# Kernel optimization log

Hardware: AMD Instinct MI355X
Metric: run time of the kernel (lower is better)

The kernel has to match this reference:

```python
import jax, jax.numpy as jnp
import numpy as np

B, C, H, W = 8, 256, 128, 128
NH, WS = 8, 8
HD = C // NH
WNH, WNW = H // WS, W // WS


def _rel_pos_index():
    coords = np.stack(np.meshgrid(np.arange(WS), np.arange(WS), indexing='ij'))  # [2,ws,ws]
    flat = coords.reshape(2, -1)
    rel = (flat[:, :, None] - flat[:, None, :]).transpose(1, 2, 0)  # [ws^2,ws^2,2]
    rel[..., 0] += WS - 1
    rel[..., 1] += WS - 1
    rel[..., 0] *= 2 * WS - 1
    return jnp.asarray(rel.sum(-1))  # [ws^2,ws^2]


def grid_sample(img, grid):
    # Bilinear, padding_mode='zeros', align_corners=True. img [N,C,H,W], grid [N,Hg,Wg,2] (x,y in [-1,1])
    N, Ci, Hi, Wi = img.shape
    gx = (grid[..., 0] + 1.0) * 0.5 * (Wi - 1)
    gy = (grid[..., 1] + 1.0) * 0.5 * (Hi - 1)
    x0 = jnp.floor(gx)
    y0 = jnp.floor(gy)
    x0i = x0.astype(jnp.int32)
    y0i = y0.astype(jnp.int32)
    wx1 = gx - x0
    wx0 = 1.0 - wx1
    wy1 = gy - y0
    wy0 = 1.0 - wy1
    nb = jnp.arange(N)[:, None, None]

    def corner(yi, xi, wgt):
        valid = (yi >= 0) & (yi < Hi) & (xi >= 0) & (xi < Wi)
        yc = jnp.clip(yi, 0, Hi - 1)
        xc = jnp.clip(xi, 0, Wi - 1)
        val = img[nb, :, yc, xc]  # [N,Hg,Wg,C]
        return val * (wgt * valid)[..., None]

    out = (corner(y0i, x0i, wy0 * wx0) + corner(y0i, x0i + 1, wy0 * wx1)
           + corner(y0i + 1, x0i, wy1 * wx0) + corner(y0i + 1, x0i + 1, wy1 * wx1))
    return jnp.transpose(out, (0, 3, 1, 2))


def setup_inputs() -> dict:
    key = jax.random.key(0)
    ks = jax.random.split(key, 10)
    f = lambda k, s, sc=1.0: jax.random.normal(k, s, dtype=jnp.float32) * sc
    return {
        'x': f(ks[0], (B, C, H, W)),
        'qkv_w': f(ks[1], (3 * C, C), 0.02),
        'qkv_b': f(ks[2], (3 * C,), 0.02),
        'bias_w': f(ks[3], (2 * NH, C), 0.02),
        'bias_b': f(ks[4], (2 * NH,), 0.02),
        'scale_w': f(ks[5], (2 * NH, C), 0.02),
        'scale_b': f(ks[6], (2 * NH,), 0.02),
        'proj_w': f(ks[7], (C, C), 0.02),
        'proj_b': f(ks[8], (C,), 0.02),
        'rpb_table': f(ks[9], ((2 * WS - 1) ** 2, NH), 0.02),
    }


def reference(x, qkv_w, qkv_b, bias_w, bias_b, scale_w, scale_b, proj_w, proj_b, rpb_table):
    scale = HD ** -0.5
    N = B * NH
    # ---- deterministic base sampling coordinates (shift=0, no padding since H,W % WS == 0) ----
    lin_w = jnp.linspace(-1.0, 1.0, W)
    lin_h = jnp.linspace(-1.0, 1.0, H)
    winref_w = lin_w.reshape(WNW, WS).mean(-1)  # window centers along width
    winref_h = lin_h.reshape(WNH, WS).mean(-1)
    off_w = jnp.arange(WS) * 2.0 / (W - 1)
    off_w = off_w - off_w.mean()
    off_h = jnp.arange(WS) * 2.0 / (H - 1)
    off_h = off_h - off_h.mean()
    base_x = jnp.broadcast_to(winref_w[None, None, :, None] + off_w[None, None, None, :], (WNH, WS, WNW, WS))
    base_y = jnp.broadcast_to((winref_h[:, None] + off_h[None, :])[:, :, None, None], (WNH, WS, WNW, WS))
    # ---- predicted per-head per-window biases & scales ----
    xp = jax.nn.leaky_relu(x.reshape(B, C, WNH, WS, WNW, WS).mean((3, 5)))  # [B,C,WNH,WNW]
    biases = (jnp.einsum('oc,bchw->bohw', bias_w, xp) + bias_b[None, :, None, None]).reshape(N, 2, WNH, WNW)
    bx = biases[:, 0] / WNW  # sampling_biases[:,0] / (w // ws)
    by = biases[:, 1] / WNH
    scales = (jnp.einsum('oc,bchw->bohw', scale_w, xp) + scale_b[None, :, None, None]).reshape(N, 2, WNH, WNW)
    sx, sy = scales[:, 0], scales[:, 1]
    # final = base + local_offsets * scale + bias (broadcast [N,WNH,1,WNW,1] over window interior)
    cx = base_x[None] + off_w[None, None, None, None, :] * sx[:, :, None, :, None] + bx[:, :, None, :, None]
    cy = base_y[None] + off_h[None, None, :, None, None] * sy[:, :, None, :, None] + by[:, :, None, :, None]
    grid = jnp.stack([cx, cy], -1).reshape(N, H, W, 2)
    # ---- qkv via 1x1 conv ----
    qkv = (jnp.einsum('oc,bchw->bohw', qkv_w, x) + qkv_b[None, :, None, None]).reshape(B, 3, NH, HD, H, W)
    q = qkv[:, 0].reshape(N, HD, H, W)
    k = qkv[:, 1].reshape(N, HD, H, W)
    v = qkv[:, 2].reshape(N, HD, H, W)
    ksamp = grid_sample(k, grid)
    vsamp = grid_sample(v, grid)

    def win(t):  # [N,HD,H,W] -> [B, nWin, NH, WS*WS, HD]
        t = t.reshape(B, NH, HD, WNH, WS, WNW, WS)
        return jnp.transpose(t, (0, 3, 5, 1, 4, 6, 2)).reshape(B, WNH * WNW, NH, WS * WS, HD)

    qw, kw, vw = win(q), win(ksamp), win(vsamp)
    rpb = jnp.transpose(rpb_table[_rel_pos_index().reshape(-1)].reshape(WS * WS, WS * WS, NH), (2, 0, 1))
    attn = jnp.einsum('bwhqd,bwhkd->bwhqk', qw, kw) * scale + rpb[None, None]
    attn = jax.nn.softmax(attn, axis=-1)
    out = jnp.einsum('bwhqk,bwhkd->bwhqd', attn, vw)
    out = out.reshape(B, WNH, WNW, NH, WS, WS, HD)
    out = jnp.transpose(out, (0, 3, 6, 1, 4, 2, 5)).reshape(B, C, H, W)
    out = jnp.einsum('oc,bchw->bohw', proj_w, out) + proj_b[None, :, None, None]
    return out
```

## Files before the change

kernel.cpp:

```cpp
#include <hip/hip_runtime.h>
#include <hip/hip_fp16.h>

#define B_ 8
#define C_ 256
#define H_ 128
#define W_ 128
#define NH_ 8
#define WS_ 8
#define HD_ 32
#define WN_ 16
#define NWIN_ 256
#define HW_ 16384

typedef unsigned short ushort_t;
typedef unsigned int uint_t;
typedef __attribute__((ext_vector_type(8))) short short8;
typedef _Float16 __attribute__((ext_vector_type(8))) half8;
typedef __attribute__((ext_vector_type(4))) float f32x4;

__device__ __forceinline__ ushort_t bf16_rtn(float x) {
    uint_t u = __float_as_uint(x);
    return (ushort_t)((u + 0x7FFFu + ((u >> 16) & 1u)) >> 16);
}
__device__ __forceinline__ uint_t bfpack(float a, float b) {
    return (uint_t)bf16_rtn(a) | ((uint_t)bf16_rtn(b) << 16);
}
__device__ __forceinline__ uint_t h2pack(float a, float b) {
    __half2 h = __floats2half2_rn(a, b);
    return __builtin_bit_cast(uint_t, h);
}

__global__ __launch_bounds__(256) void wconv_kernel(const float* __restrict__ w,
                            ushort_t* __restrict__ wh, int n4) {
    int i = blockIdx.x*256 + threadIdx.x;
    if (i >= n4) return;
    float4 v = ((const float4*)w)[i];
    ((uint2*)wh)[i] = make_uint2(bfpack(v.x, v.y), bfpack(v.z, v.w));
}

__global__ __launch_bounds__(256) void rpb_expand_kernel(const float* __restrict__ rpb_table,
                            float* __restrict__ rpbT) {
    int nh = blockIdx.x;
    int t = threadIdx.x;
    #pragma unroll
    for (int rr = 0; rr < 16; ++rr) {
        int e = t*16 + rr;
        int kcol = e >> 6, qrow = e & 63;
        int yq = qrow >> 3, xq = qrow & 7, yk = kcol >> 3, xk = kcol & 7;
        int idx = (yq - yk + 7)*15 + (xq - xk + 7);
        rpbT[((size_t)nh*64 + kcol)*64 + qrow] = rpb_table[idx*8 + nh];
    }
}

__global__ __launch_bounds__(256) void transpose_split_kernel(const float* __restrict__ x,
                            ushort_t* __restrict__ th, float* __restrict__ xpart) {
    __shared__ float tile[64][65];
    int b = blockIdx.z;
    int p0 = blockIdx.x * 64, c0 = blockIdx.y * 64;
    const float* xsrc = x + (size_t)b*C_*HW_;
    int t = threadIdx.x;
    #pragma unroll
    for (int r = 0; r < 4; ++r) {
        int task = t + r*256;
        int cl = task >> 4, p4 = (task & 15) * 4;
        float4 v = *(const float4*)(xsrc + (size_t)(c0+cl)*HW_ + p0 + p4);
        tile[cl][p4+0] = v.x; tile[cl][p4+1] = v.y; tile[cl][p4+2] = v.z; tile[cl][p4+3] = v.w;
    }
    __syncthreads();
    {
        int h = blockIdx.x >> 1, wbase = (blockIdx.x & 1) * 8;
        #pragma unroll
        for (int r = 0; r < 2; ++r) {
            int task = t + r*256;
            int cl = task >> 3, wx = task & 7;
            float s = 0.f;
            #pragma unroll
            for (int j = 0; j < 8; ++j) s += tile[cl][wx*8+j];
            xpart[(((size_t)b*256 + c0+cl)*128 + h)*16 + wbase + wx] = s;
        }
    }
    ushort_t* thb = th + (size_t)b*HW_*256;
    #pragma unroll
    for (int r = 0; r < 2; ++r) {
        int task = t + r*256;
        int pl = task >> 3, cb = (task & 7) * 8;
        uint4 Hh;
        Hh.x = bfpack(tile[cb+0][pl], tile[cb+1][pl]);
        Hh.y = bfpack(tile[cb+2][pl], tile[cb+3][pl]);
        Hh.z = bfpack(tile[cb+4][pl], tile[cb+5][pl]);
        Hh.w = bfpack(tile[cb+6][pl], tile[cb+7][pl]);
        *(uint4*)(thb + (size_t)(p0+pl)*256 + c0 + cb) = Hh;
    }
}

__global__ __launch_bounds__(256) void pool2_kernel(const float* __restrict__ xpart, float* __restrict__ xp) {
    int bc = blockIdx.x;
    int t = threadIdx.x;
    int wy = t >> 4, wxg = t & 15;
    const float* src = xpart + (size_t)bc*2048;
    float s = 0.f;
    #pragma unroll
    for (int i = 0; i < 8; ++i) s += src[(wy*8+i)*16 + wxg];
    s *= (1.f/64.f);
    xp[(size_t)bc*256 + t] = s > 0.f ? s : 0.01f*s;
}

__global__ __launch_bounds__(256) void params_kernel(const float* __restrict__ xp,
                              const float* __restrict__ bias_w, const float* __restrict__ bias_b,
                              const float* __restrict__ scale_w, const float* __restrict__ scale_b,
                              float* __restrict__ params) {
    __shared__ float xs[256];
    int blk = blockIdx.x;
    int b = blk >> 8, win = blk & 255;
    int t = threadIdx.x;
    xs[t] = xp[((size_t)(b*256 + t))*256 + win];
    __syncthreads();
    if (t < 32) {
        int which = t >> 4;
        int o = t & 15;
        const float* Wm = which ? scale_w : bias_w;
        float acc = which ? scale_b[o] : bias_b[o];
        for (int c = 0; c < 256; ++c) acc += Wm[o*256 + c] * xs[c];
        int nh = o >> 1, comp = o & 1;
        int n = b*8 + nh;
        float v = which ? acc : 3.96875f * acc;
        params[((size_t)(n*256 + win))*4 + which*2 + comp] = v;
    }
}

__global__ __launch_bounds__(256) void mgemm_qkvt_kernel(const ushort_t* __restrict__ wq,
                            const ushort_t* __restrict__ xt,
                            const float* __restrict__ bias,
                            ushort_t* __restrict__ qt, ushort_t* __restrict__ kv) {
    __shared__ __align__(16) uint4 smem[2112];
    uint4* Ah = smem; uint4* Bh = smem + 1024;
    int zb = blockIdx.z;
    const ushort_t* xh = xt + (size_t)zb*HW_*256;
    ushort_t* qtb = qt + (size_t)zb*HW_*256;
    ushort_t* kvb = kv + (size_t)zb*8*HW_*64;
    int o0 = blockIdx.x * 128, p0 = blockIdx.y * 128;
    int t = threadIdx.x;
    int lane = t & 63, wid = t >> 6;
    int wm = wid >> 1, wn = wid & 1;
    int q = lane >> 4, rl = lane & 15;

    f32x4 acc[4][4];
    #pragma unroll
    for (int f = 0; f < 4; ++f)
        #pragma unroll
        for (int g = 0; g < 4; ++g)
            acc[f][g] = (f32x4){0.f, 0.f, 0.f, 0.f};

    int srow = t >> 1, shalf = t & 1;
    int sw = srow & 7;

    for (int ks = 0; ks < 4; ++ks) {
        int c0 = ks * 64;
        __syncthreads();
        {
            const uint4* a_h = (const uint4*)(wq + (size_t)(o0+srow)*256 + c0);
            const uint4* b_h = (const uint4*)(xh + (size_t)(p0+srow)*256 + c0);
            #pragma unroll
            for (int jj = 0; jj < 4; ++jj) {
                int u = shalf*4 + jj;
                int d = srow*8 + (u ^ sw);
                Ah[d] = a_h[u]; Bh[d] = b_h[u];
            }
        }
        __syncthreads();
        #pragma unroll
        for (int kk = 0; kk < 2; ++kk) {
            short8 afh[4], bfh[4];
            #pragma unroll
            for (int f = 0; f < 4; ++f) {
                int row = wm*64 + f*16 + rl;
                int u = (kk*4 + q) ^ (row & 7);
                afh[f] = __builtin_bit_cast(short8, Ah[row*8 + u]);
            }
            #pragma unroll
            for (int g = 0; g < 4; ++g) {
                int row = wn*64 + g*16 + rl;
                int u = (kk*4 + q) ^ (row & 7);
                bfh[g] = __builtin_bit_cast(short8, Bh[row*8 + u]);
            }
            #pragma unroll
            for (int f = 0; f < 4; ++f)
                #pragma unroll
                for (int g = 0; g < 4; ++g)
                    acc[f][g] = __builtin_amdgcn_mfma_f32_16x16x32_bf16(afh[f], bfh[g], acc[f][g], 0, 0, 0);
        }
    }
    float* tb = (float*)smem;
    int pl = t >> 1, half = t & 1;
    #pragma unroll
    for (int pass = 0; pass < 2; ++pass) {
        __syncthreads();
        if (wm == pass) {
            #pragma unroll
            for (int f = 0; f < 4; ++f)
                #pragma unroll
                for (int g = 0; g < 4; ++g)
                    #pragma unroll
                    for (int r = 0; r < 4; ++r)
                        tb[(f*16 + q*4 + r)*129 + wn*64 + g*16 + rl] = acc[f][g][r];
        }
        __syncthreads();
        {
            int obase = o0 + pass*64 + half*32;
            int type = obase >> 8;
            int oo = obase & 255;
            int head = oo >> 5;
            size_t pix = p0 + pl;
            ushort_t* dst = (type == 0)
                ? qtb + pix*256 + oo
                : kvb + ((size_t)head*HW_ + pix)*64 + ((type == 2) ? 32 : 0) + (oo & 31);
            #pragma unroll
            for (int u = 0; u < 4; ++u) {
                float v[8];
                #pragma unroll
                for (int e = 0; e < 8; ++e) v[e] = tb[(half*32 + u*8 + e)*129 + pl];
                float4 b0 = *(const float4*)&bias[obase + u*8];
                float4 b1 = *(const float4*)&bias[obase + u*8 + 4];
                uint4 Hv;
                Hv.x = h2pack(v[0]+b0.x, v[1]+b0.y);
                Hv.y = h2pack(v[2]+b0.z, v[3]+b0.w);
                Hv.z = h2pack(v[4]+b1.x, v[5]+b1.y);
                Hv.w = h2pack(v[6]+b1.z, v[7]+b1.w);
                *(uint4*)(dst + u*8) = Hv;
            }
        }
    }
}

__global__ __launch_bounds__(256) void mgemm_proj_kernel(const ushort_t* __restrict__ wp,
                            const ushort_t* __restrict__ at,
                            const float* __restrict__ bias, float* __restrict__ out) {
    __shared__ __align__(16) uint4 smem[2048];
    uint4* Ah = smem; uint4* Bh = smem + 1024;
    int zb = blockIdx.z;
    const ushort_t* xh = at + (size_t)zb*HW_*256;
    float* outb = out + (size_t)zb*C_*HW_;
    int o0 = blockIdx.x * 128, p0 = blockIdx.y * 128;
    int t = threadIdx.x;
    int lane = t & 63, wid = t >> 6;
    int wm = wid >> 1, wn = wid & 1;
    int q = lane >> 4, rl = lane & 15;

    f32x4 acc[4][4];
    #pragma unroll
    for (int f = 0; f < 4; ++f)
        #pragma unroll
        for (int g = 0; g < 4; ++g)
            acc[f][g] = (f32x4){0.f, 0.f, 0.f, 0.f};

    int srow = t >> 1, shalf = t & 1;
    int sw = srow & 7;

    for (int ks = 0; ks < 4; ++ks) {
        int c0 = ks * 64;
        __syncthreads();
        {
            const uint4* a_h = (const uint4*)(wp + (size_t)(o0+srow)*256 + c0);
            const uint4* b_h = (const uint4*)(xh + (size_t)(p0+srow)*256 + c0);
            #pragma unroll
            for (int jj = 0; jj < 4; ++jj) {
                int u = shalf*4 + jj;
                int d = srow*8 + (u ^ sw);
                Ah[d] = a_h[u]; Bh[d] = b_h[u];
            }
        }
        __syncthreads();
        #pragma unroll
        for (int kk = 0; kk < 2; ++kk) {
            short8 afh[4], bfh[4];
            #pragma unroll
            for (int f = 0; f < 4; ++f) {
                int row = wm*64 + f*16 + rl;
                int u = (kk*4 + q) ^ (row & 7);
                afh[f] = __builtin_bit_cast(short8, Ah[row*8 + u]);
            }
            #pragma unroll
            for (int g = 0; g < 4; ++g) {
                int row = wn*64 + g*16 + rl;
                int u = (kk*4 + q) ^ (row & 7);
                bfh[g] = __builtin_bit_cast(short8, Bh[row*8 + u]);
            }
            #pragma unroll
            for (int f = 0; f < 4; ++f)
                #pragma unroll
                for (int g = 0; g < 4; ++g)
                    acc[f][g] = __builtin_amdgcn_mfma_f32_16x16x32_bf16(afh[f], bfh[g], acc[f][g], 0, 0, 0);
        }
    }
    #pragma unroll
    for (int f = 0; f < 4; ++f) {
        float4 bb = *(const float4*)&bias[o0 + wm*64 + f*16 + q*4];
        float bbv[4] = {bb.x, bb.y, bb.z, bb.w};
        #pragma unroll
        for (int g = 0; g < 4; ++g) {
            int p = p0 + wn*64 + g*16 + rl;
            #pragma unroll
            for (int r = 0; r < 4; ++r) {
                int o = o0 + wm*64 + f*16 + q*4 + r;
                outb[(size_t)o*HW_ + p] = acc[f][g][r] + bbv[r];
            }
        }
    }
}

__global__ __launch_bounds__(256) void attn_kernel(const ushort_t* __restrict__ qt,
                            const ushort_t* __restrict__ kv,
                            const float* __restrict__ params_,
                            const float* __restrict__ rpbT,
                            ushort_t* __restrict__ at) {
    __shared__ __align__(16) ushort_t smem[64*40 + 64*40 + 32*72 + 64*40];
    ushort_t (*Q_lds)[40]   = (ushort_t(*)[40])smem;
    ushort_t (*K_lds)[40]   = (ushort_t(*)[40])(smem + 2560);
    ushort_t (*VT_lds)[72]  = (ushort_t(*)[72])(smem + 5120);
    ushort_t (*P_lds)[72]   = (ushort_t(*)[72])smem;
    ushort_t (*OUT_lds)[40] = (ushort_t(*)[40])(smem + 5120 + 2304);

    int b = blockIdx.y;
    int blk = blockIdx.x;
    int win = blk >> 3, nh = blk & 7;
    int wy = win >> 4, wx = win & 15;
    int t = threadIdx.x;
    int lane = t & 63, wid = t >> 6;

    const float* pp = params_ + ((size_t)((b*8 + nh)*256 + win))*4;
    float ox = pp[0], oy = pp[1], sx = pp[2], sy = pp[3];

    const ushort_t* qtb = qt + (size_t)b*HW_*256;
    const ushort_t* kvb = kv + ((size_t)(b*8 + nh))*HW_*64;
    ushort_t* ath = at + (size_t)b*HW_*256;

    {
        int tok = t >> 2, cg = t & 3;
        int i = tok >> 3, j = tok & 7;
        size_t pix = (size_t)(wy*8 + i)*W_ + wx*8 + j;
        *(uint4*)&Q_lds[tok][cg*8] = *(const uint4*)(qtb + pix*256 + nh*32 + cg*8);
    }
    {
        int tokq = lane >> 3, sub = lane & 7;
        #pragma unroll
        for (int r = 0; r < 2; ++r) {
            int tok = wid*16 + r*8 + tokq;
            int i = tok >> 3, j = tok & 7;
            int h = wy*8 + i, wpx = wx*8 + j;
            float gx = (float)wpx + ((float)j - 3.5f)*sx + ox;
            float gy = (float)h  + ((float)i - 3.5f)*sy + oy;
            float x0f = floorf(gx), y0f = floorf(gy);
            int x0 = (int)x0f, y0 = (int)y0f;
            float wx1 = gx - x0f, wy1 = gy - y0f;
            float wxz = 1.f - wx1, wyz = 1.f - wy1;
            int x1 = x0 + 1, y1 = y0 + 1;
            float m00 = wyz*wxz * ((y0>=0 && y0<H_ && x0>=0 && x0<W_) ? 1.f : 0.f);
            float m01 = wyz*wx1 * ((y0>=0 && y0<H_ && x1>=0 && x1<W_) ? 1.f : 0.f);
            float m10 = wy1*wxz * ((y1>=0 && y1<H_ && x0>=0 && x0<W_) ? 1.f : 0.f);
            float m11 = wy1*wx1 * ((y1>=0 && y1<H_ && x1>=0 && x1<W_) ? 1.f : 0.f);
            int x0c = min(max(x0,0),W_-1), x1c = min(max(x1,0),W_-1);
            int y0c = min(max(y0,0),H_-1), y1c = min(max(y1,0),H_-1);
            size_t p00 = (size_t)y0c*W_ + x0c, p01 = (size_t)y0c*W_ + x1c;
            size_t p10 = (size_t)y1c*W_ + x0c, p11 = (size_t)y1c*W_ + x1c;
            __half2 a0 = __float2half2_rn(0.f), a1 = a0, a2 = a0, a3 = a0;
            #define CORNER(PIX, M) { \
                uint4 u = *(const uint4*)(kvb + (PIX)*64 + sub*8); \
                __half2 wv = __float2half2_rn(M); \
                a0 = __hfma2(__builtin_bit_cast(__half2, u.x), wv, a0); \
                a1 = __hfma2(__builtin_bit_cast(__half2, u.y), wv, a1); \
                a2 = __hfma2(__builtin_bit_cast(__half2, u.z), wv, a2); \
                a3 = __hfma2(__builtin_bit_cast(__half2, u.w), wv, a3); }
            CORNER(p00, m00)
            CORNER(p01, m01)
            CORNER(p10, m10)
            CORNER(p11, m11)
            #undef CORNER
            if (sub < 4) {
                uint4 Kv;
                Kv.x = __builtin_bit_cast(uint_t, a0); Kv.y = __builtin_bit_cast(uint_t, a1);
                Kv.z = __builtin_bit_cast(uint_t, a2); Kv.w = __builtin_bit_cast(uint_t, a3);
                *(uint4*)&K_lds[tok][sub*8] = Kv;
            } else {
                int d0 = (sub - 4)*8;
                VT_lds[d0+0][tok] = __half_as_ushort(__low2half(a0));
                VT_lds[d0+1][tok] = __half_as_ushort(__high2half(a0));
                VT_lds[d0+2][tok] = __half_as_ushort(__low2half(a1));
                VT_lds[d0+3][tok] = __half_as_ushort(__high2half(a1));
                VT_lds[d0+4][tok] = __half_as_ushort(__low2half(a2));
                VT_lds[d0+5][tok] = __half_as_ushort(__high2half(a2));
                VT_lds[d0+6][tok] = __half_as_ushort(__low2half(a3));
                VT_lds[d0+7][tok] = __half_as_ushort(__high2half(a3));
            }
        }
    }
    __syncthreads();

    int q = lane >> 4, rl = lane & 15;
    const float scale = 0.17677669529663687f;

    half8 a_frag = *(const half8*)&Q_lds[wid*16 + rl][q*8];
    half8 b_frag[4];
    #pragma unroll
    for (int g = 0; g < 4; ++g)
        b_frag[g] = *(const half8*)&K_lds[g*16 + rl][q*8];
    __syncthreads();

    f32x4 accS[4];
    #pragma unroll
    for (int g = 0; g < 4; ++g)
        accS[g] = __builtin_amdgcn_mfma_f32_16x16x32_f16(a_frag, b_frag[g], (f32x4){0.f,0.f,0.f,0.f}, 0, 0, 0);

    float Sv[4][4];
    const float* rpbb = rpbT + (size_t)nh*4096;
    int m0 = wid*16 + q*4;
    #pragma unroll
    for (int g = 0; g < 4; ++g) {
        float4 rv = *(const float4*)&rpbb[(g*16 + rl)*64 + m0];
        Sv[g][0] = accS[g][0]*scale + rv.x;
        Sv[g][1] = accS[g][1]*scale + rv.y;
        Sv[g][2] = accS[g][2]*scale + rv.z;
        Sv[g][3] = accS[g][3]*scale + rv.w;
    }
    float inv[4];
    #pragma unroll
    for (int r = 0; r < 4; ++r) {
        float pm = fmaxf(fmaxf(Sv[0][r], Sv[1][r]), fmaxf(Sv[2][r], Sv[3][r]));
        pm = fmaxf(pm, __shfl_xor(pm, 1));
        pm = fmaxf(pm, __shfl_xor(pm, 2));
        pm = fmaxf(pm, __shfl_xor(pm, 4));
        pm = fmaxf(pm, __shfl_xor(pm, 8));
        float s = 0.f;
        #pragma unroll
        for (int g = 0; g < 4; ++g) {
            float e = __expf(Sv[g][r] - pm);
            Sv[g][r] = e;
            s += e;
        }
        s += __shfl_xor(s, 1);
        s += __shfl_xor(s, 2);
        s += __shfl_xor(s, 4);
        s += __shfl_xor(s, 8);
        inv[r] = 1.f / s;
    }
    #pragma unroll
    for (int r = 0; r < 4; ++r) {
        int m = wid*16 + q*4 + r;
        #pragma unroll
        for (int g = 0; g < 4; ++g)
            P_lds[m][g*16 + rl] = __half_as_ushort(__float2half(Sv[g][r]*inv[r]));
    }

    f32x4 accO[2] = {(f32x4){0.f,0.f,0.f,0.f}, (f32x4){0.f,0.f,0.f,0.f}};
    #pragma unroll
    for (int ks = 0; ks < 2; ++ks) {
        half8 p_frag = *(const half8*)&P_lds[wid*16 + rl][ks*32 + q*8];
        #pragma unroll
        for (int g2 = 0; g2 < 2; ++g2) {
            half8 v_frag = *(const half8*)&VT_lds[g2*16 + rl][ks*32 + q*8];
            accO[g2] = __builtin_amdgcn_mfma_f32_16x16x32_f16(p_frag, v_frag, accO[g2], 0, 0, 0);
        }
    }
    #pragma unroll
    for (int r = 0; r < 4; ++r) {
        int m = wid*16 + q*4 + r;
        OUT_lds[m][rl]      = bf16_rtn(accO[0][r]);
        OUT_lds[m][16 + rl] = bf16_rtn(accO[1][r]);
    }
    __syncthreads();
    {
        int tok = t >> 2, cg = t & 3;
        int i2 = tok >> 3, j2 = tok & 7;
        size_t pix = (size_t)(wy*8 + i2)*W_ + wx*8 + j2;
        *(uint4*)(ath + pix*256 + nh*32 + cg*8) = *(const uint4*)&OUT_lds[tok][cg*8];
    }
}

extern "C" void kernel_launch(void* const* d_in, const int* in_sizes, int n_in,
                              void* d_out, int out_size, void* d_ws, size_t ws_size,
                              hipStream_t stream) {
    const float* x       = (const float*)d_in[0];
    const float* qkv_w   = (const float*)d_in[1];
    const float* qkv_b   = (const float*)d_in[2];
    const float* bias_w  = (const float*)d_in[3];
    const float* bias_b  = (const float*)d_in[4];
    const float* scale_w = (const float*)d_in[5];
    const float* scale_b = (const float*)d_in[6];
    const float* proj_w  = (const float*)d_in[7];
    const float* proj_b  = (const float*)d_in[8];
    const float* rpb     = (const float*)d_in[9];
    float* out = (float*)d_out;

    char* ws = (char*)d_ws;
    float*    xp       = (float*)ws;     ws += (size_t)524288*4;
    float*    params   = (float*)ws;     ws += (size_t)65536*4;
    float*    xpart    = (float*)ws;     ws += (size_t)4194304*4;
    float*    rpbT     = (float*)ws;     ws += (size_t)8*4096*4;
    ushort_t* wq       = (ushort_t*)ws;  ws += (size_t)768*256*2;
    ushort_t* wp       = (ushort_t*)ws;  ws += (size_t)256*256*2;
    ushort_t* xt       = (ushort_t*)ws;  ws += (size_t)B_*HW_*256*2;
    ushort_t* at       = (ushort_t*)ws;  ws += (size_t)B_*HW_*256*2;
    ushort_t* qt       = (ushort_t*)ws;  ws += (size_t)B_*HW_*256*2;
    ushort_t* kv       = (ushort_t*)ws;

    wconv_kernel<<<dim3(192), 256, 0, stream>>>(qkv_w, wq, 768*256/4);
    wconv_kernel<<<dim3(64),  256, 0, stream>>>(proj_w, wp, 256*256/4);
    rpb_expand_kernel<<<dim3(NH_), 256, 0, stream>>>(rpb, rpbT);
    transpose_split_kernel<<<dim3(256, 4, B_), 256, 0, stream>>>(x, xt, xpart);
    pool2_kernel <<<dim3(B_*C_), 256, 0, stream>>>(xpart, xp);
    params_kernel<<<dim3(B_*NWIN_), 256, 0, stream>>>(xp, bias_w, bias_b, scale_w, scale_b, params);
    mgemm_qkvt_kernel<<<dim3(6, 128, B_), 256, 0, stream>>>(wq, xt, qkv_b, qt, kv);
    attn_kernel<<<dim3(NH_*NWIN_, B_), 256, 0, stream>>>(qt, kv, params, rpbT, at);
    mgemm_proj_kernel<<<dim3(2, 128, B_), 256, 0, stream>>>(wp, at, proj_b, out);
}
```

Measured before the change: 361.0 us.

## Fuse x transpose and pooling partials into QKV GEMM with fp16 operands

```diff
diff --git a/kernel.cpp b/kernel.cpp
--- a/kernel.cpp
+++ b/kernel.cpp
@@ -30,6 +30,14 @@
     return __builtin_bit_cast(uint_t, h);
 }
 
+__global__ __launch_bounds__(256) void wconv_h_kernel(const float* __restrict__ w,
+                            ushort_t* __restrict__ wh, int n4) {
+    int i = blockIdx.x*256 + threadIdx.x;
+    if (i >= n4) return;
+    float4 v = ((const float4*)w)[i];
+    ((uint2*)wh)[i] = make_uint2(h2pack(v.x, v.y), h2pack(v.z, v.w));
+}
+
 __global__ __launch_bounds__(256) void wconv_kernel(const float* __restrict__ w,
                             ushort_t* __restrict__ wh, int n4) {
     int i = blockIdx.x*256 + threadIdx.x;
@@ -49,47 +57,6 @@
         int yq = qrow >> 3, xq = qrow & 7, yk = kcol >> 3, xk = kcol & 7;
         int idx = (yq - yk + 7)*15 + (xq - xk + 7);
         rpbT[((size_t)nh*64 + kcol)*64 + qrow] = rpb_table[idx*8 + nh];
-    }
-}
-
-__global__ __launch_bounds__(256) void transpose_split_kernel(const float* __restrict__ x,
-                            ushort_t* __restrict__ th, float* __restrict__ xpart) {
-    __shared__ float tile[64][65];
-    int b = blockIdx.z;
-    int p0 = blockIdx.x * 64, c0 = blockIdx.y * 64;
-    const float* xsrc = x + (size_t)b*C_*HW_;
-    int t = threadIdx.x;
-    #pragma unroll
-    for (int r = 0; r < 4; ++r) {
-        int task = t + r*256;
-        int cl = task >> 4, p4 = (task & 15) * 4;
-        float4 v = *(const float4*)(xsrc + (size_t)(c0+cl)*HW_ + p0 + p4);
-        tile[cl][p4+0] = v.x; tile[cl][p4+1] = v.y; tile[cl][p4+2] = v.z; tile[cl][p4+3] = v.w;
-    }
-    __syncthreads();
-    {
-        int h = blockIdx.x >> 1, wbase = (blockIdx.x & 1) * 8;
-        #pragma unroll
-        for (int r = 0; r < 2; ++r) {
-            int task = t + r*256;
-            int cl = task >> 3, wx = task & 7;
-            float s = 0.f;
-            #pragma unroll
-            for (int j = 0; j < 8; ++j) s += tile[cl][wx*8+j];
-            xpart[(((size_t)b*256 + c0+cl)*128 + h)*16 + wbase + wx] = s;
-        }
-    }
-    ushort_t* thb = th + (size_t)b*HW_*256;
-    #pragma unroll
-    for (int r = 0; r < 2; ++r) {
-        int task = t + r*256;
-        int pl = task >> 3, cb = (task & 7) * 8;
-        uint4 Hh;
-        Hh.x = bfpack(tile[cb+0][pl], tile[cb+1][pl]);
-        Hh.y = bfpack(tile[cb+2][pl], tile[cb+3][pl]);
-        Hh.z = bfpack(tile[cb+4][pl], tile[cb+5][pl]);
-        Hh.w = bfpack(tile[cb+6][pl], tile[cb+7][pl]);
-        *(uint4*)(thb + (size_t)(p0+pl)*256 + c0 + cb) = Hh;
     }
 }
 
@@ -128,17 +95,21 @@
     }
 }
 
-__global__ __launch_bounds__(256) void mgemm_qkvt_kernel(const ushort_t* __restrict__ wq,
-                            const ushort_t* __restrict__ xt,
+__global__ __launch_bounds__(256) void mgemm_qkvx_kernel(const ushort_t* __restrict__ wq,
+                            const float* __restrict__ x,
                             const float* __restrict__ bias,
-                            ushort_t* __restrict__ qt, ushort_t* __restrict__ kv) {
-    __shared__ __align__(16) uint4 smem[2112];
-    uint4* Ah = smem; uint4* Bh = smem + 1024;
+                            ushort_t* __restrict__ qt, ushort_t* __restrict__ kv,
+                            float* __restrict__ xpart) {
+    __shared__ __align__(16) uint4 Albuf[1024];
+    __shared__ __align__(16) float Btile[64*129];
+    uint4* B16 = (uint4*)Btile;
+
     int zb = blockIdx.z;
-    const ushort_t* xh = xt + (size_t)zb*HW_*256;
+    const float* xb = x + (size_t)zb*C_*HW_;
     ushort_t* qtb = qt + (size_t)zb*HW_*256;
     ushort_t* kvb = kv + (size_t)zb*8*HW_*64;
     int o0 = blockIdx.x * 128, p0 = blockIdx.y * 128;
+    int hrow = blockIdx.y;
     int t = threadIdx.x;
     int lane = t & 63, wid = t >> 6;
     int wm = wid >> 1, wn = wid & 1;
@@ -159,38 +130,76 @@
         __syncthreads();
         {
             const uint4* a_h = (const uint4*)(wq + (size_t)(o0+srow)*256 + c0);
-            const uint4* b_h = (const uint4*)(xh + (size_t)(p0+srow)*256 + c0);
             #pragma unroll
             for (int jj = 0; jj < 4; ++jj) {
                 int u = shalf*4 + jj;
-                int d = srow*8 + (u ^ sw);
-                Ah[d] = a_h[u]; Bh[d] = b_h[u];
-            }
+                Albuf[srow*8 + (u ^ sw)] = a_h[u];
+            }
+        }
+        {
+            #pragma unroll
+            for (int r = 0; r < 8; ++r) {
+                int task = t + r*256;
+                int cl = task >> 5, p4 = (task & 31) * 4;
+                float4 v = *(const float4*)(xb + (size_t)(c0+cl)*HW_ + p0 + p4);
+                float* dst = &Btile[cl*129 + p4];
+                dst[0] = v.x; dst[1] = v.y; dst[2] = v.z; dst[3] = v.w;
+            }
+        }
+        __syncthreads();
+        if (blockIdx.x == 0) {
+            #pragma unroll
+            for (int r = 0; r < 4; ++r) {
+                int task = t + r*256;
+                int cl = task >> 4, wxg = task & 15;
+                float s = 0.f;
+                #pragma unroll
+                for (int j = 0; j < 8; ++j) s += Btile[cl*129 + wxg*8 + j];
+                xpart[(((size_t)zb*256 + c0+cl)*128 + hrow)*16 + wxg] = s;
+            }
+        }
+        uint4 cvt[4];
+        #pragma unroll
+        for (int r = 0; r < 4; ++r) {
+            int task = t + r*256;
+            int pl = task >> 3, cb = (task & 7) * 8;
+            float f[8];
+            #pragma unroll
+            for (int e = 0; e < 8; ++e) f[e] = Btile[(cb+e)*129 + pl];
+            cvt[r].x = h2pack(f[0], f[1]); cvt[r].y = h2pack(f[2], f[3]);
+            cvt[r].z = h2pack(f[4], f[5]); cvt[r].w = h2pack(f[6], f[7]);
+        }
+        __syncthreads();
+        #pragma unroll
+        for (int r = 0; r < 4; ++r) {
+            int task = t + r*256;
+            int pl = task >> 3, u = task & 7;
+            B16[pl*8 + (u ^ (pl & 7))] = cvt[r];
         }
         __syncthreads();
         #pragma unroll
         for (int kk = 0; kk < 2; ++kk) {
-            short8 afh[4], bfh[4];
+            half8 afh[4], bfh[4];
             #pragma unroll
             for (int f = 0; f < 4; ++f) {
                 int row = wm*64 + f*16 + rl;
                 int u = (kk*4 + q) ^ (row & 7);
-                afh[f] = __builtin_bit_cast(short8, Ah[row*8 + u]);
+                afh[f] = __builtin_bit_cast(half8, Albuf[row*8 + u]);
             }
             #pragma unroll
             for (int g = 0; g < 4; ++g) {
                 int row = wn*64 + g*16 + rl;
                 int u = (kk*4 + q) ^ (row & 7);
-                bfh[g] = __builtin_bit_cast(short8, Bh[row*8 + u]);
+                bfh[g] = __builtin_bit_cast(half8, B16[row*8 + u]);
             }
             #pragma unroll
             for (int f = 0; f < 4; ++f)
                 #pragma unroll
                 for (int g = 0; g < 4; ++g)
-                    acc[f][g] = __builtin_amdgcn_mfma_f32_16x16x32_bf16(afh[f], bfh[g], acc[f][g], 0, 0, 0);
-        }
-    }
-    float* tb = (float*)smem;
+                    acc[f][g] = __builtin_amdgcn_mfma_f32_16x16x32_f16(afh[f], bfh[g], acc[f][g], 0, 0, 0);
+        }
+    }
+    float* tb = Btile;
     int pl = t >> 1, half = t & 1;
     #pragma unroll
     for (int pass = 0; pass < 2; ++pass) {
@@ -497,18 +506,16 @@
     float*    rpbT     = (float*)ws;     ws += (size_t)8*4096*4;
     ushort_t* wq       = (ushort_t*)ws;  ws += (size_t)768*256*2;
     ushort_t* wp       = (ushort_t*)ws;  ws += (size_t)256*256*2;
-    ushort_t* xt       = (ushort_t*)ws;  ws += (size_t)B_*HW_*256*2;
     ushort_t* at       = (ushort_t*)ws;  ws += (size_t)B_*HW_*256*2;
     ushort_t* qt       = (ushort_t*)ws;  ws += (size_t)B_*HW_*256*2;
     ushort_t* kv       = (ushort_t*)ws;
 
-    wconv_kernel<<<dim3(192), 256, 0, stream>>>(qkv_w, wq, 768*256/4);
-    wconv_kernel<<<dim3(64),  256, 0, stream>>>(proj_w, wp, 256*256/4);
+    wconv_h_kernel<<<dim3(192), 256, 0, stream>>>(qkv_w, wq, 768*256/4);
+    wconv_kernel  <<<dim3(64),  256, 0, stream>>>(proj_w, wp, 256*256/4);
     rpb_expand_kernel<<<dim3(NH_), 256, 0, stream>>>(rpb, rpbT);
-    transpose_split_kernel<<<dim3(256, 4, B_), 256, 0, stream>>>(x, xt, xpart);
+    mgemm_qkvx_kernel<<<dim3(6, 128, B_), 256, 0, stream>>>(wq, x, qkv_b, qt, kv, xpart);
     pool2_kernel <<<dim3(B_*C_), 256, 0, stream>>>(xpart, xp);
     params_kernel<<<dim3(B_*NWIN_), 256, 0, stream>>>(xp, bias_w, bias_b, scale_w, scale_b, params);
-    mgemm_qkvt_kernel<<<dim3(6, 128, B_), 256, 0, stream>>>(wq, xt, qkv_b, qt, kv);
     attn_kernel<<<dim3(NH_*NWIN_, B_), 256, 0, stream>>>(qt, kv, params, rpbT, at);
     mgemm_proj_kernel<<<dim3(2, 128, B_), 256, 0, stream>>>(wp, at, proj_b, out);
 }
```

Result: no change. 362.2 us (+0.3%).

## Pre-pack QKV weights in MFMA fragment order and load A directly from global

Applied to the files above, without the earlier changes.

```diff
diff --git a/kernel.cpp b/kernel.cpp
--- a/kernel.cpp
+++ b/kernel.cpp
@@ -28,6 +28,26 @@
 __device__ __forceinline__ uint_t h2pack(float a, float b) {
     __half2 h = __floats2half2_rn(a, b);
     return __builtin_bit_cast(uint_t, h);
+}
+
+__global__ __launch_bounds__(256) void wpack_kernel(const float* __restrict__ w,
+                            ushort_t* __restrict__ wpk) {
+    int u = blockIdx.x*256 + threadIdx.x;
+    int lane = u & 63;
+    int f    = (u >> 6) & 3;
+    int kk   = (u >> 8) & 1;
+    int ks   = (u >> 9) & 3;
+    int wm   = (u >> 11) & 1;
+    int oc   = u >> 12;
+    int o = oc*128 + wm*64 + f*16 + (lane & 15);
+    int c = ks*64 + kk*32 + (lane >> 4)*8;
+    const float* src = w + (size_t)o*256 + c;
+    float4 v0 = *(const float4*)src;
+    float4 v1 = *(const float4*)(src + 4);
+    uint4 Hv;
+    Hv.x = bfpack(v0.x, v0.y); Hv.y = bfpack(v0.z, v0.w);
+    Hv.z = bfpack(v1.x, v1.y); Hv.w = bfpack(v1.z, v1.w);
+    ((uint4*)wpk)[u] = Hv;
 }
 
 __global__ __launch_bounds__(256) void wconv_kernel(const float* __restrict__ w,
@@ -128,21 +148,25 @@
     }
 }
 
-__global__ __launch_bounds__(256) void mgemm_qkvt_kernel(const ushort_t* __restrict__ wq,
+__global__ __launch_bounds__(256) void mgemm_qkvt2_kernel(const ushort_t* __restrict__ wpk,
                             const ushort_t* __restrict__ xt,
                             const float* __restrict__ bias,
                             ushort_t* __restrict__ qt, ushort_t* __restrict__ kv) {
-    __shared__ __align__(16) uint4 smem[2112];
-    uint4* Ah = smem; uint4* Bh = smem + 1024;
+    __shared__ __align__(16) float smem_f[64*67];
+    uint4* Bh = (uint4*)smem_f;
+    float* tb = smem_f;
     int zb = blockIdx.z;
+    int oc = blockIdx.x;
+    int o0 = oc * 128, p0 = blockIdx.y * 128;
     const ushort_t* xh = xt + (size_t)zb*HW_*256;
     ushort_t* qtb = qt + (size_t)zb*HW_*256;
     ushort_t* kvb = kv + (size_t)zb*8*HW_*64;
-    int o0 = blockIdx.x * 128, p0 = blockIdx.y * 128;
     int t = threadIdx.x;
     int lane = t & 63, wid = t >> 6;
     int wm = wid >> 1, wn = wid & 1;
-    int q = lane >> 4, rl = lane & 15;
+    int qi = lane >> 4, rl = lane & 15;
+
+    const ushort_t* wpkA = wpk + (size_t)(oc*2 + wm)*16384;
 
     f32x4 acc[4][4];
     #pragma unroll
@@ -155,32 +179,27 @@
     int sw = srow & 7;
 
     for (int ks = 0; ks < 4; ++ks) {
-        int c0 = ks * 64;
         __syncthreads();
         {
-            const uint4* a_h = (const uint4*)(wq + (size_t)(o0+srow)*256 + c0);
-            const uint4* b_h = (const uint4*)(xh + (size_t)(p0+srow)*256 + c0);
+            const uint4* src = (const uint4*)(xh + (size_t)(p0+srow)*256 + ks*64);
             #pragma unroll
             for (int jj = 0; jj < 4; ++jj) {
                 int u = shalf*4 + jj;
-                int d = srow*8 + (u ^ sw);
-                Ah[d] = a_h[u]; Bh[d] = b_h[u];
+                Bh[srow*8 + (u ^ sw)] = src[u];
             }
         }
         __syncthreads();
         #pragma unroll
         for (int kk = 0; kk < 2; ++kk) {
             short8 afh[4], bfh[4];
-            #pragma unroll
-            for (int f = 0; f < 4; ++f) {
-                int row = wm*64 + f*16 + rl;
-                int u = (kk*4 + q) ^ (row & 7);
-                afh[f] = __builtin_bit_cast(short8, Ah[row*8 + u]);
-            }
+            const ushort_t* wk = wpkA + ((ks*2 + kk)*4)*512 + lane*8;
+            #pragma unroll
+            for (int f = 0; f < 4; ++f)
+                afh[f] = *(const short8*)(wk + f*512);
             #pragma unroll
             for (int g = 0; g < 4; ++g) {
                 int row = wn*64 + g*16 + rl;
-                int u = (kk*4 + q) ^ (row & 7);
+                int u = (kk*4 + qi) ^ (row & 7);
                 bfh[g] = __builtin_bit_cast(short8, Bh[row*8 + u]);
             }
             #pragma unroll
@@ -190,43 +209,45 @@
                     acc[f][g] = __builtin_amdgcn_mfma_f32_16x16x32_bf16(afh[f], bfh[g], acc[f][g], 0, 0, 0);
         }
     }
-    float* tb = (float*)smem;
-    int pl = t >> 1, half = t & 1;
-    #pragma unroll
-    for (int pass = 0; pass < 2; ++pass) {
-        __syncthreads();
-        if (wm == pass) {
-            #pragma unroll
-            for (int f = 0; f < 4; ++f)
+    #pragma unroll
+    for (int pm = 0; pm < 2; ++pm) {
+        #pragma unroll
+        for (int pn = 0; pn < 2; ++pn) {
+            __syncthreads();
+            if (wm == pm && wn == pn) {
                 #pragma unroll
-                for (int g = 0; g < 4; ++g)
+                for (int f = 0; f < 4; ++f)
                     #pragma unroll
-                    for (int r = 0; r < 4; ++r)
-                        tb[(f*16 + q*4 + r)*129 + wn*64 + g*16 + rl] = acc[f][g][r];
-        }
-        __syncthreads();
-        {
-            int obase = o0 + pass*64 + half*32;
-            int type = obase >> 8;
-            int oo = obase & 255;
-            int head = oo >> 5;
-            size_t pix = p0 + pl;
-            ushort_t* dst = (type == 0)
-                ? qtb + pix*256 + oo
-                : kvb + ((size_t)head*HW_ + pix)*64 + ((type == 2) ? 32 : 0) + (oo & 31);
-            #pragma unroll
-            for (int u = 0; u < 4; ++u) {
-                float v[8];
+                    for (int g = 0; g < 4; ++g)
+                        #pragma unroll
+                        for (int r = 0; r < 4; ++r)
+                            tb[(f*16 + qi*4 + r)*67 + g*16 + rl] = acc[f][g][r];
+            }
+            __syncthreads();
+            {
+                int pxl = t >> 2, cg = t & 3;
+                size_t pix = p0 + pn*64 + pxl;
+                int obase = o0 + pm*64 + cg*16;
+                int type = obase >> 8;
+                int oo = obase & 255;
+                int head = oo >> 5;
+                ushort_t* dst = (type == 0)
+                    ? qtb + pix*256 + oo
+                    : kvb + ((size_t)head*HW_ + pix)*64 + ((type == 2) ? 32 : 0) + (oo & 31);
+                float v[16];
                 #pragma unroll
-                for (int e = 0; e < 8; ++e) v[e] = tb[(half*32 + u*8 + e)*129 + pl];
-                float4 b0 = *(const float4*)&bias[obase + u*8];
-                float4 b1 = *(const float4*)&bias[obase + u*8 + 4];
-                uint4 Hv;
-                Hv.x = h2pack(v[0]+b0.x, v[1]+b0.y);
-                Hv.y = h2pack(v[2]+b0.z, v[3]+b0.w);
-                Hv.z = h2pack(v[4]+b1.x, v[5]+b1.y);
-                Hv.w = h2pack(v[6]+b1.z, v[7]+b1.w);
-                *(uint4*)(dst + u*8) = Hv;
+                for (int e = 0; e < 16; ++e) v[e] = tb[(cg*16 + e)*67 + pxl];
+                float4 b0 = *(const float4*)&bias[obase];
+                float4 b1 = *(const float4*)&bias[obase + 4];
+                float4 b2 = *(const float4*)&bias[obase + 8];
+                float4 b3 = *(const float4*)&bias[obase + 12];
+                uint4 H0, H1;
+                H0.x = h2pack(v[0]+b0.x,  v[1]+b0.y);  H0.y = h2pack(v[2]+b0.z,  v[3]+b0.w);
+                H0.z = h2pack(v[4]+b1.x,  v[5]+b1.y);  H0.w = h2pack(v[6]+b1.z,  v[7]+b1.w);
+                H1.x = h2pack(v[8]+b2.x,  v[9]+b2.y);  H1.y = h2pack(v[10]+b2.z, v[11]+b2.w);
+                H1.z = h2pack(v[12]+b3.x, v[13]+b3.y); H1.w = h2pack(v[14]+b3.z, v[15]+b3.w);
+                *(uint4*)dst = H0;
+                *(uint4*)(dst + 8) = H1;
             }
         }
     }
@@ -495,20 +516,20 @@
     float*    params   = (float*)ws;     ws += (size_t)65536*4;
     float*    xpart    = (float*)ws;     ws += (size_t)4194304*4;
     float*    rpbT     = (float*)ws;     ws += (size_t)8*4096*4;
-    ushort_t* wq       = (ushort_t*)ws;  ws += (size_t)768*256*2;
+    ushort_t* wpk      = (ushort_t*)ws;  ws += (size_t)768*256*2;
     ushort_t* wp       = (ushort_t*)ws;  ws += (size_t)256*256*2;
     ushort_t* xt       = (ushort_t*)ws;  ws += (size_t)B_*HW_*256*2;
     ushort_t* at       = (ushort_t*)ws;  ws += (size_t)B_*HW_*256*2;
     ushort_t* qt       = (ushort_t*)ws;  ws += (size_t)B_*HW_*256*2;
     ushort_t* kv       = (ushort_t*)ws;
 
-    wconv_kernel<<<dim3(192), 256, 0, stream>>>(qkv_w, wq, 768*256/4);
-    wconv_kernel<<<dim3(64),  256, 0, stream>>>(proj_w, wp, 256*256/4);
+    wpack_kernel<<<dim3(96), 256, 0, stream>>>(qkv_w, wpk);
+    wconv_kernel<<<dim3(64), 256, 0, stream>>>(proj_w, wp, 256*256/4);
     rpb_expand_kernel<<<dim3(NH_), 256, 0, stream>>>(rpb, rpbT);
     transpose_split_kernel<<<dim3(256, 4, B_), 256, 0, stream>>>(x, xt, xpart);
     pool2_kernel <<<dim3(B_*C_), 256, 0, stream>>>(xpart, xp);
     params_kernel<<<dim3(B_*NWIN_), 256, 0, stream>>>(xp, bias_w, bias_b, scale_w, scale_b, params);
-    mgemm_qkvt_kernel<<<dim3(6, 128, B_), 256, 0, stream>>>(wq, xt, qkv_b, qt, kv);
+    mgemm_qkvt2_kernel<<<dim3(6, 128, B_), 256, 0, stream>>>(wpk, xt, qkv_b, qt, kv);
     attn_kernel<<<dim3(NH_*NWIN_, B_), 256, 0, stream>>>(qt, kv, params, rpbT, at);
     mgemm_proj_kernel<<<dim3(2, 128, B_), 256, 0, stream>>>(wp, at, proj_b, out);
 }
```

After: 362.5 us. No clear change (+0.4%).
